# Kernel optimization log

Measured on AMD Instinct MI355X. Metric: run time of the kernel, lower is better.

## Reference

```python
import jax, jax.numpy as jnp
import numpy as np

B, T, C, H, S, M = 4, 4096, 1024, 16, 256, 32
D = C // H  # size_head = 64


def setup_inputs() -> dict:
    key = jax.random.key(0)
    ks = jax.random.split(key, 10)
    scale = 1.0 / (C * C)
    return {
        "x_q": jax.random.normal(ks[0], (B, T, C), dtype=jnp.float32),
        "x_r": jax.random.normal(ks[1], (B, T, C), dtype=jnp.float32),
        "y": jax.random.normal(ks[2], (B, T, C), dtype=jnp.float32),
        "Wi": jax.random.normal(ks[3], (C, C), dtype=jnp.float32) * 0.02,
        "bi": jnp.zeros((C,), jnp.float32),
        "Ws": jax.random.normal(ks[4], (S, D), dtype=jnp.float32) * 0.02,
        "bs": jnp.zeros((S,), jnp.float32),
        "temp": jnp.ones((1, H, 1, 1), jnp.float32) / jnp.sqrt(jnp.float32(D)),
        "w_re": jax.random.uniform(ks[5], (H, D, D, M), dtype=jnp.float32) * scale,
        "w_im": jax.random.uniform(ks[6], (H, D, D, M), dtype=jnp.float32) * scale,
        "Wo": jax.random.normal(ks[7], (C, C), dtype=jnp.float32) * 0.02,
        "bo": jnp.zeros((C,), jnp.float32),
    }


def reference(x_q, x_r, y, Wi, bi, Ws, bs, temp, w_re, w_im, Wo, bo):
    b, t, c = x_q.shape
    d = c // H
    # in_proj -> [B, H, T, D]
    tmp = (x_q @ Wi.T + bi).reshape(b, t, H, d).transpose(0, 2, 1, 3)
    # slice logits [B, H, T, S], scaled by learned temperature
    logits = (tmp @ Ws.T + bs) / temp
    # softmax over tokens (n): slice-attention pooling to S virtual points
    z = jnp.einsum('bhnc,bhns->bhsc', tmp, jax.nn.softmax(logits, axis=-2))
    z = z.transpose(0, 1, 3, 2)  # [B, H, D, S]
    n = z.shape[-1]
    z_fft = jnp.fft.rfft(z)  # [B, H, D, S//2+1]
    w = (w_re + 1j * w_im).astype(z_fft.dtype)
    out_m = jnp.einsum('bhix,hiox->bhox', z_fft[..., :M], w)  # [B, H, D, M]
    out_ft = jnp.zeros((b, H, d, n // 2 + 1), dtype=out_m.dtype).at[..., :M].set(out_m)
    out = jnp.fft.irfft(out_ft, n=n)  # [B, H, D, S]
    out = out.transpose(0, 1, 3, 2)  # [B, H, S, D]
    # softmax over slices (g): scatter back to tokens
    out = jnp.einsum('bhgc,bhng->bhnc', out, jax.nn.softmax(logits, axis=-1))
    out = out.transpose(0, 2, 1, 3).reshape(b, t, c)  # merge heads
    return out @ Wo.T + bo
```

## Files before the change

kernel.cpp:

```cpp
#include <hip/hip_runtime.h>
#include <hip/hip_bf16.h>

typedef __attribute__((ext_vector_type(8))) _Float16 half8;
typedef __attribute__((ext_vector_type(4))) _Float16 half4;
typedef __attribute__((ext_vector_type(4))) float f32x4;

#define DEVFN __device__ __forceinline__

constexpr int B_ = 4, T_ = 4096, C_ = 1024, H_ = 16, S_ = 256, M_ = 32, D_ = 64;
constexpr int NT_ = B_ * T_;
constexpr float FSCALE = 65536.0f;
constexpr float TWOPI = 6.283185307179586f;

DEVFN half8 cvt8(const float4 a, const float4 b) {
  half8 h;
  h[0] = (_Float16)a.x; h[1] = (_Float16)a.y; h[2] = (_Float16)a.z; h[3] = (_Float16)a.w;
  h[4] = (_Float16)b.x; h[5] = (_Float16)b.y; h[6] = (_Float16)b.z; h[7] = (_Float16)b.w;
  return h;
}

#define GLD16(gsrc, ldst)                                                        \
  __builtin_amdgcn_global_load_lds(                                              \
      (const __attribute__((address_space(1))) uint32_t*)(gsrc),                 \
      (__attribute__((address_space(3))) uint32_t*)(ldst), 16, 0, 0)

__global__ void k_diag(float* __restrict__ out, float wsz) {
  if (threadIdx.x == 0 && blockIdx.x == 0) out[0] = wsz;
}

__global__ void kw_cvt(const float* __restrict__ src, _Float16* __restrict__ dst, int n) {
  const int i = (blockIdx.x * blockDim.x + threadIdx.x) * 8;
  if (i < n) {
    float4 a = ((const float4*)(src + i))[0];
    float4 b = ((const float4*)(src + i))[1];
    *(half8*)(dst + i) = cvt8(a, b);
  }
}

__global__ void k0_prep(const float* __restrict__ Ws, const float* __restrict__ bs,
                        const float* __restrict__ temp,
                        _Float16* __restrict__ Wsh, float* __restrict__ bsh) {
  const int h = blockIdx.x;
  const int tid = threadIdx.x;
  const float invt = 1.0f / temp[h];
  for (int i = tid; i < S_ * D_; i += 256)
    Wsh[(size_t)h * S_ * D_ + i] = (_Float16)(Ws[i] * invt);
  if (tid < S_) bsh[h * S_ + tid] = bs[tid] * invt;
}

__global__ __launch_bounds__(256) void k1_in_proj(
    const _Float16* __restrict__ Xh, const _Float16* __restrict__ Wih, const float* __restrict__ bi,
    _Float16* __restrict__ tmp_h, _Float16* __restrict__ tmp_hT)
{
  __shared__ _Float16 As[128 * 32];
  __shared__ _Float16 Bs[128 * 32];
  const int tid = threadIdx.x;
  const int orig = blockIdx.y * gridDim.x + blockIdx.x;
  const int wgid = (orig & 7) * 128 + (orig >> 3);
  const int rowBase = (wgid >> 3) * 128;
  const int colBase = (wgid & 7) * 128;
  const int w = tid >> 6, lane = tid & 63;
  const int wr = w >> 1, wc = w & 1;
  const int fr = lane & 15, fg = lane >> 4;
  const int srow0 = w * 16 + (lane >> 2);
  const int srow1 = (4 + w) * 16 + (lane >> 2);
  const int scol  = (lane & 3) * 8;
  const size_t arow0 = (size_t)(rowBase + srow0) * C_ + scol;
  const size_t arow1 = (size_t)(rowBase + srow1) * C_ + scol;
  const size_t brow0 = (size_t)(colBase + srow0) * C_ + scol;
  const size_t brow1 = (size_t)(colBase + srow1) * C_ + scol;
  f32x4 acc[4][4] = {};
  for (int kt = 0; kt < C_; kt += 32) {
    __syncthreads();
    GLD16(Xh  + arow0 + kt, &As[w * 512]);
    GLD16(Xh  + arow1 + kt, &As[(4 + w) * 512]);
    GLD16(Wih + brow0 + kt, &Bs[w * 512]);
    GLD16(Wih + brow1 + kt, &Bs[(4 + w) * 512]);
    __syncthreads();
    half8 a[4], b[4];
#pragma unroll
    for (int i = 0; i < 4; ++i) a[i] = *(const half8*)&As[(wr * 64 + i * 16 + fr) * 32 + fg * 8];
#pragma unroll
    for (int j = 0; j < 4; ++j) b[j] = *(const half8*)&Bs[(wc * 64 + j * 16 + fr) * 32 + fg * 8];
#pragma unroll
    for (int i = 0; i < 4; ++i)
#pragma unroll
      for (int j = 0; j < 4; ++j)
        acc[i][j] = __builtin_amdgcn_mfma_f32_16x16x32_f16(a[i], b[j], acc[i][j], 0, 0, 0);
  }
#pragma unroll
  for (int i = 0; i < 4; ++i) {
#pragma unroll
    for (int j = 0; j < 4; ++j) {
      const int col = colBase + wc * 64 + j * 16 + fr;
      const int hh = col >> 6, d = col & 63;
      const float bv = bi[col];
      const int g0 = rowBase + wr * 64 + i * 16 + fg * 4;
      const int bb = g0 >> 12;
      const int t0 = g0 & (T_ - 1);
      half4 pk;
#pragma unroll
      for (int r = 0; r < 4; ++r) {
        const _Float16 hv = (_Float16)(acc[i][j][r] + bv);
        tmp_h[(((size_t)(bb * H_ + hh)) * T_ + t0 + r) * D_ + d] = hv;
        pk[r] = hv;
      }
      *(half4*)&tmp_hT[(((size_t)(bb * H_ + hh)) * D_ + d) * T_ + t0] = pk;
    }
  }
}

__global__ __launch_bounds__(256) void k3_pool(
    const _Float16* __restrict__ tmp_h, const _Float16* __restrict__ tmp_hT,
    const _Float16* __restrict__ Wsh, const float* __restrict__ bsh,
    float* __restrict__ Zpart, float* __restrict__ rowsum, float* __restrict__ colsumP)
{
  __shared__ _Float16 Es[256][72];
  __shared__ _Float16 Bt[64][72];
  __shared__ float red[64][4];
  const int tid = threadIdx.x;
  const int kc = blockIdx.x;
  const int bh = blockIdx.y;
  const int hh = bh & (H_ - 1);
  const int w = tid >> 6, lane = tid & 63;
  const int fr = lane & 15, fg = lane >> 4;
  const size_t tmpB  = (size_t)bh * T_ * D_;
  const size_t tmpTB = (size_t)bh * D_ * T_;
  const _Float16* WshH = Wsh + (size_t)hh * S_ * D_;
  float bsreg[4];
#pragma unroll
  for (int nj = 0; nj < 4; ++nj) bsreg[nj] = bsh[hh * S_ + w * 64 + nj * 16 + fr];
  f32x4 acc2[4][4] = {};
  float cacc[4] = {0.f, 0.f, 0.f, 0.f};
  const int brow = tid >> 2, bc0 = (tid & 3) * 16;
  for (int step = 0; step < 8; ++step) {
    const int t0 = kc * 512 + step * 64;
    {
      const _Float16* src = tmp_hT + tmpTB + (size_t)brow * T_ + t0 + bc0;
      *(half8*)&Bt[brow][bc0]     = ((const half8*)src)[0];
      *(half8*)&Bt[brow][bc0 + 8] = ((const half8*)src)[1];
    }
    f32x4 acc1[4][4] = {};
#pragma unroll
    for (int ks = 0; ks < 2; ++ks) {
      half8 a[4], b[4];
#pragma unroll
      for (int mi = 0; mi < 4; ++mi)
        a[mi] = *(const half8*)(tmp_h + tmpB + (size_t)(t0 + mi * 16 + fr) * D_ + ks * 32 + fg * 8);
#pragma unroll
      for (int nj = 0; nj < 4; ++nj)
        b[nj] = *(const half8*)(WshH + (size_t)(w * 64 + nj * 16 + fr) * D_ + ks * 32 + fg * 8);
#pragma unroll
      for (int mi = 0; mi < 4; ++mi)
#pragma unroll
        for (int nj = 0; nj < 4; ++nj)
          acc1[mi][nj] = __builtin_amdgcn_mfma_f32_16x16x32_f16(a[mi], b[nj], acc1[mi][nj], 0, 0, 0);
    }
#pragma unroll
    for (int mi = 0; mi < 4; ++mi) {
      float rsp[4] = {0.f, 0.f, 0.f, 0.f};
#pragma unroll
      for (int nj = 0; nj < 4; ++nj) {
        half4 p;
        float csp = 0.f;
#pragma unroll
        for (int r = 0; r < 4; ++r) {
          const float e = __expf(acc1[mi][nj][r] + bsreg[nj]);
          p[r] = (_Float16)e;
          rsp[r] += e;
          csp += e;
        }
        cacc[nj] += csp;
        *(half4*)&Es[w * 64 + nj * 16 + fr][mi * 16 + fg * 4] = p;
      }
#pragma unroll
      for (int r = 0; r < 4; ++r) {
        float v = rsp[r];
        v += __shfl_xor(v, 1); v += __shfl_xor(v, 2);
        v += __shfl_xor(v, 4); v += __shfl_xor(v, 8);
        if (fr == 0) red[mi * 16 + fg * 4 + r][w] = v;
      }
    }
    __syncthreads();
#pragma unroll
    for (int kt = 0; kt < 2; ++kt) {
      half8 a2[4], b2[4];
#pragma unroll
      for (int mi = 0; mi < 4; ++mi) a2[mi] = *(const half8*)&Es[w * 64 + mi * 16 + fr][kt * 32 + fg * 8];
#pragma unroll
      for (int nj = 0; nj < 4; ++nj) b2[nj] = *(const half8*)&Bt[nj * 16 + fr][kt * 32 + fg * 8];
#pragma unroll
      for (int mi = 0; mi < 4; ++mi)
#pragma unroll
        for (int nj = 0; nj < 4; ++nj)
          acc2[mi][nj] = __builtin_amdgcn_mfma_f32_16x16x32_f16(a2[mi], b2[nj], acc2[mi][nj], 0, 0, 0);
    }
    if (tid < 64)
      rowsum[(size_t)bh * T_ + t0 + tid] = red[tid][0] + red[tid][1] + red[tid][2] + red[tid][3];
    __syncthreads();
  }
#pragma unroll
  for (int nj = 0; nj < 4; ++nj) {
    float v = cacc[nj];
    v += __shfl_xor(v, 16); v += __shfl_xor(v, 32);
    if (fg == 0) colsumP[((size_t)bh * 8 + kc) * S_ + w * 64 + nj * 16 + fr] = v;
  }
#pragma unroll
  for (int mi = 0; mi < 4; ++mi)
#pragma unroll
    for (int nj = 0; nj < 4; ++nj)
#pragma unroll
      for (int r = 0; r < 4; ++r)
        Zpart[(((size_t)bh * 8 + kc) * S_ + w * 64 + mi * 16 + fg * 4 + r) * D_ + nj * 16 + fr]
            = acc2[mi][nj][r];
}

__global__ __launch_bounds__(256) void k4a_dft(
    const float* __restrict__ Zpart, const float* __restrict__ colsumP,
    float* __restrict__ Fre, float* __restrict__ Fim)
{
  __shared__ float zsh[256][17];
  __shared__ float csh[256];
  __shared__ float tc[256], ts[256];
  const int tid = threadIdx.x;
  const int ic = blockIdx.x;
  const int bh = blockIdx.y;
  {
    const float ang = (float)tid * (TWOPI / 256.0f);
    tc[tid] = cosf(ang); ts[tid] = sinf(ang);
    float c = 0.f;
#pragma unroll
    for (int kc = 0; kc < 8; ++kc) c += colsumP[((size_t)bh * 8 + kc) * S_ + tid];
    csh[tid] = c;
  }
  __syncthreads();
  for (int idx = tid; idx < 256 * 16; idx += 256) {
    const int s = idx >> 4, dd = idx & 15;
    float v = 0.f;
#pragma unroll
    for (int kc = 0; kc < 8; ++kc)
      v += Zpart[(((size_t)bh * 8 + kc) * S_ + s) * D_ + ic * 16 + dd];
    zsh[s][dd] = v / csh[s];
  }
  __syncthreads();
  const int ii = tid >> 4;
  const int mh = tid & 15;
#pragma unroll
  for (int q = 0; q < 2; ++q) {
    const int m = mh + 16 * q;
    float re = 0.f, im = 0.f;
    int k = 0;
    for (int s = 0; s < 256; ++s) {
      const float zv = zsh[s][ii];
      re += zv * tc[k];
      im -= zv * ts[k];
      k = (k + m) & 255;
    }
    Fre[((size_t)bh * D_ + ic * 16 + ii) * M_ + m] = re;
    Fim[((size_t)bh * D_ + ic * 16 + ii) * M_ + m] = im;
  }
}

__global__ __launch_bounds__(256) void k4b_mix(
    const float* __restrict__ Fre, const float* __restrict__ Fim,
    const float* __restrict__ w_re, const float* __restrict__ w_im,
    _Float16* __restrict__ fout_T)
{
  __shared__ _Float16 Fsr[4][64][33];
  __shared__ _Float16 Fsi[4][64][33];
  __shared__ float Gpre[2][4][4][32];
  __shared__ float Gpim[2][4][4][32];
  __shared__ float Gre[4][4][32];
  __shared__ float Gim[4][4][32];
  __shared__ float tc[256], ts[256];
  const int tid = threadIdx.x;
  const int oc = blockIdx.x;
  const int h  = blockIdx.y;
  for (int idx = tid; idx < 4 * 64 * 32; idx += 256) {
    const int b = idx >> 11, rem = idx & 2047, i = rem >> 5, m = rem & 31;
    const size_t off = ((size_t)(b * 16 + h) * D_ + i) * M_ + m;
    Fsr[b][i][m] = (_Float16)Fre[off];
    Fsi[b][i][m] = (_Float16)Fim[off];
  }
  {
    const float ang = (float)tid * (TWOPI / 256.0f);
    tc[tid] = cosf(ang); ts[tid] = sinf(ang);
  }
  __syncthreads();
  {
    const int ih = tid >> 7, o = (tid >> 5) & 3, m = tid & 31;
    float gre[4] = {0,0,0,0}, gim[4] = {0,0,0,0};
    for (int i = ih * 32; i < ih * 32 + 32; ++i) {
      const size_t wo = (((size_t)h * D_ + i) * D_ + oc * 4 + o) * M_ + m;
      const float wre = w_re[wo], wim = w_im[wo];
#pragma unroll
      for (int b = 0; b < 4; ++b) {
        const float fre = (float)Fsr[b][i][m], fim = (float)Fsi[b][i][m];
        gre[b] += fre * wre - fim * wim;
        gim[b] += fre * wim + fim * wre;
      }
    }
#pragma unroll
    for (int b = 0; b < 4; ++b) { Gpre[ih][b][o][m] = gre[b]; Gpim[ih][b][o][m] = gim[b]; }
  }
  __syncthreads();
  for (int idx = tid; idx < 512; idx += 256) {
    const int b = idx >> 7, o = (idx >> 5) & 3, m = idx & 31;
    Gre[b][o][m] = Gpre[0][b][o][m] + Gpre[1][b][o][m];
    Gim[b][o][m] = Gpim[0][b][o][m] + Gpim[1][b][o][m];
  }
  __syncthreads();
  {
    const int b = tid >> 6, o = (tid >> 4) & 3, sc = tid & 15;
    for (int s5 = 0; s5 < 16; ++s5) {
      const int s = sc * 16 + s5;
      float v = Gre[b][o][0];
      int km = s;
#pragma unroll
      for (int m = 1; m < 32; ++m) {
        v += 2.0f * (Gre[b][o][m] * tc[km] - Gim[b][o][m] * ts[km]);
        km = (km + s) & 255;
      }
      fout_T[((size_t)(b * 16 + h) * D_ + oc * 4 + o) * S_ + s] = (_Float16)(v * (FSCALE / 256.0f));
    }
  }
}

__global__ __launch_bounds__(256) void k5_scatter(
    const _Float16* __restrict__ Wsh, const float* __restrict__ bsh,
    const _Float16* __restrict__ fout_T, const float* __restrict__ rowsum,
    _Float16* __restrict__ tmp_io)
{
  __shared__ _Float16 Fs[64][264];
  __shared__ _Float16 Es[64][264];
  __shared__ float bshl[256];
  const int tid = threadIdx.x;
  const int orig = blockIdx.y * gridDim.x + blockIdx.x;
  const int nidx = (orig & 7) * 64 + (orig >> 3);
  const int bh = nidx >> 3;
  const int tcn = nidx & 7;
  const int hh = bh & (H_ - 1);
  const int w = tid >> 6, lane = tid & 63;
  const int fr = lane & 15, fg = lane >> 4;
  {
    const int row = tid >> 2, c0 = (tid & 3) * 64;
    const _Float16* src = fout_T + (size_t)bh * D_ * S_ + (size_t)row * S_ + c0;
#pragma unroll
    for (int q = 0; q < 8; ++q)
      *(half8*)&Fs[row][c0 + q * 8] = ((const half8*)src)[q];
  }
  bshl[tid] = bsh[hh * S_ + tid];
  __syncthreads();
  const _Float16* WshH = Wsh + (size_t)hh * S_ * D_;
  const size_t tmpB = (size_t)bh * T_ * D_ + (size_t)tcn * 512 * D_;
  const int trow = w * 16 + fr;
  half8 bf0, bf1;
  {
    const _Float16* p = tmp_io + tmpB + (size_t)trow * D_ + fg * 8;
    bf0 = *(const half8*)p;
    bf1 = *(const half8*)(p + 32);
  }
  for (int step = 0; step < 8; ++step) {
    {
      f32x4 acc1[8];
#pragma unroll
      for (int mi = 0; mi < 8; ++mi) acc1[mi] = (f32x4){0.f, 0.f, 0.f, 0.f};
#pragma unroll
      for (int mi = 0; mi < 8; ++mi) {
        const half8 a0 = *(const half8*)(WshH + (size_t)(mi * 16 + fr) * D_ + fg * 8);
        acc1[mi] = __builtin_amdgcn_mfma_f32_16x16x32_f16(a0, bf0, acc1[mi], 0, 0, 0);
      }
#pragma unroll
      for (int mi = 0; mi < 8; ++mi) {
        const half8 a1 = *(const half8*)(WshH + (size_t)(mi * 16 + fr) * D_ + 32 + fg * 8);
        acc1[mi] = __builtin_amdgcn_mfma_f32_16x16x32_f16(a1, bf1, acc1[mi], 0, 0, 0);
      }
#pragma unroll
      for (int mi = 0; mi < 8; ++mi) {
        const float4 bv = *(const float4*)&bshl[mi * 16 + fg * 4];
        half4 pk;
        pk[0] = (_Float16)__expf(acc1[mi][0] + bv.x);
        pk[1] = (_Float16)__expf(acc1[mi][1] + bv.y);
        pk[2] = (_Float16)__expf(acc1[mi][2] + bv.z);
        pk[3] = (_Float16)__expf(acc1[mi][3] + bv.w);
        *(half4*)&Es[trow][mi * 16 + fg * 4] = pk;
      }
    }
    {
      f32x4 acc1[8];
#pragma unroll
      for (int mi = 0; mi < 8; ++mi) acc1[mi] = (f32x4){0.f, 0.f, 0.f, 0.f};
#pragma unroll
      for (int mi = 0; mi < 8; ++mi) {
        const half8 a0 = *(const half8*)(WshH + (size_t)((8 + mi) * 16 + fr) * D_ + fg * 8);
        acc1[mi] = __builtin_amdgcn_mfma_f32_16x16x32_f16(a0, bf0, acc1[mi], 0, 0, 0);
      }
#pragma unroll
      for (int mi = 0; mi < 8; ++mi) {
        const half8 a1 = *(const half8*)(WshH + (size_t)((8 + mi) * 16 + fr) * D_ + 32 + fg * 8);
        acc1[mi] = __builtin_amdgcn_mfma_f32_16x16x32_f16(a1, bf1, acc1[mi], 0, 0, 0);
      }
#pragma unroll
      for (int mi = 0; mi < 8; ++mi) {
        const float4 bv = *(const float4*)&bshl[(8 + mi) * 16 + fg * 4];
        half4 pk;
        pk[0] = (_Float16)__expf(acc1[mi][0] + bv.x);
        pk[1] = (_Float16)__expf(acc1[mi][1] + bv.y);
        pk[2] = (_Float16)__expf(acc1[mi][2] + bv.z);
        pk[3] = (_Float16)__expf(acc1[mi][3] + bv.w);
        *(half4*)&Es[trow][(8 + mi) * 16 + fg * 4] = pk;
      }
    }
    if (step < 7) {
      const _Float16* p = tmp_io + tmpB + (size_t)((step + 1) * 64 + trow) * D_ + fg * 8;
      bf0 = *(const half8*)p;
      bf1 = *(const half8*)(p + 32);
    }
    f32x4 acc2[4];
#pragma unroll
    for (int nj = 0; nj < 4; ++nj) acc2[nj] = (f32x4){0.f, 0.f, 0.f, 0.f};
#pragma unroll
    for (int ks = 0; ks < 8; ++ks) {
      const half8 ea = *(const half8*)&Es[w * 16 + fr][ks * 32 + fg * 8];
#pragma unroll
      for (int nj = 0; nj < 4; ++nj) {
        const half8 fb = *(const half8*)&Fs[nj * 16 + fr][ks * 32 + fg * 8];
        acc2[nj] = __builtin_amdgcn_mfma_f32_16x16x32_f16(ea, fb, acc2[nj], 0, 0, 0);
      }
    }
    const int tbase = tcn * 512 + step * 64 + w * 16 + fg * 4;
    const float4 rs = *(const float4*)&rowsum[(size_t)bh * T_ + tbase];
    const float ri[4] = {1.0f / rs.x, 1.0f / rs.y, 1.0f / rs.z, 1.0f / rs.w};
#pragma unroll
    for (int r = 0; r < 4; ++r) {
      _Float16* dst = tmp_io + (size_t)bh * T_ * D_ + (size_t)(tbase + r) * D_ + fr;
#pragma unroll
      for (int nj = 0; nj < 4; ++nj)
        dst[nj * 16] = (_Float16)(acc2[nj][r] * ri[r]);
    }
  }
}

__global__ __launch_bounds__(256) void k6_out_proj(
    const _Float16* __restrict__ OT, const _Float16* __restrict__ Woh, const float* __restrict__ bo,
    float* __restrict__ Y)
{
  __shared__ _Float16 As[128 * 32];
  __shared__ _Float16 Bs[128 * 32];
  const int tid = threadIdx.x;
  const int orig = blockIdx.y * gridDim.x + blockIdx.x;
  const int wgid = (orig & 7) * 128 + (orig >> 3);
  const int rowBase = (wgid >> 3) * 128;
  const int colBase = (wgid & 7) * 128;
  const int w = tid >> 6, lane = tid & 63;
  const int wr = w >> 1, wc = w & 1;
  const int fr = lane & 15, fg = lane >> 4;
  const int srow0 = w * 16 + (lane >> 2);
  const int srow1 = (4 + w) * 16 + (lane >> 2);
  const int scol  = (lane & 3) * 8;
  const int g0 = rowBase + srow0, g1 = rowBase + srow1;
  const int bb = g0 >> 12;
  const int t0 = g0 & (T_ - 1), t1 = g1 & (T_ - 1);
  const size_t brow0 = (size_t)(colBase + srow0) * C_ + scol;
  const size_t brow1 = (size_t)(colBase + srow1) * C_ + scol;
  f32x4 acc[4][4] = {};
  for (int kt = 0; kt < C_; kt += 32) {
    const int c0 = kt + scol;
    const int hh0 = c0 >> 6, d0 = c0 & 63;
    __syncthreads();
    GLD16(OT + (((size_t)(bb * H_ + hh0)) * T_ + t0) * D_ + d0, &As[w * 512]);
    GLD16(OT + (((size_t)(bb * H_ + hh0)) * T_ + t1) * D_ + d0, &As[(4 + w) * 512]);
    GLD16(Woh + brow0 + kt, &Bs[w * 512]);
    GLD16(Woh + brow1 + kt, &Bs[(4 + w) * 512]);
    __syncthreads();
    half8 a[4], b[4];
#pragma unroll
    for (int i = 0; i < 4; ++i) a[i] = *(const half8*)&As[(wr * 64 + i * 16 + fr) * 32 + fg * 8];
#pragma unroll
    for (int j = 0; j < 4; ++j) b[j] = *(const half8*)&Bs[(wc * 64 + j * 16 + fr) * 32 + fg * 8];
#pragma unroll
    for (int i = 0; i < 4; ++i)
#pragma unroll
      for (int j = 0; j < 4; ++j)
        acc[i][j] = __builtin_amdgcn_mfma_f32_16x16x32_f16(a[i], b[j], acc[i][j], 0, 0, 0);
  }
#pragma unroll
  for (int i = 0; i < 4; ++i) {
#pragma unroll
    for (int j = 0; j < 4; ++j) {
      const int col = colBase + wc * 64 + j * 16 + fr;
      const float bv = bo[col];
      const int g0o = rowBase + wr * 64 + i * 16 + fg * 4;
#pragma unroll
      for (int r = 0; r < 4; ++r)
        Y[(size_t)(g0o + r) * C_ + col] = acc[i][j][r] * (1.0f / FSCALE) + bv;
    }
  }
}

extern "C" void kernel_launch(void* const* d_in, const int* in_sizes, int n_in,
                              void* d_out, int out_size, void* d_ws, size_t ws_size,
                              hipStream_t stream)
{
  const float* x_q  = (const float*)d_in[0];
  const float* Wi   = (const float*)d_in[3];
  const float* bi   = (const float*)d_in[4];
  const float* Ws   = (const float*)d_in[5];
  const float* bs   = (const float*)d_in[6];
  const float* temp = (const float*)d_in[7];
  const float* w_re = (const float*)d_in[8];
  const float* w_im = (const float*)d_in[9];
  const float* Wo   = (const float*)d_in[10];
  const float* bo   = (const float*)d_in[11];
  float* Y = (float*)d_out;

  char* ws = (char*)d_ws;
  size_t off = 0;
  auto alloc = [&](size_t bytes) { size_t o = off; off += (bytes + 255) & ~(size_t)255; return o; };
  const size_t o_tmp  = alloc((size_t)NT_ * C_ * 2);
  const size_t o_Wsh  = alloc((size_t)H_ * S_ * D_ * 2);
  const size_t o_bsh  = alloc((size_t)H_ * S_ * 4);
  const size_t o_Zp   = alloc((size_t)B_ * H_ * 8 * S_ * D_ * 4);
  const size_t o_row  = alloc((size_t)B_ * H_ * T_ * 4);
  const size_t o_colP = alloc((size_t)B_ * H_ * 8 * S_ * 4);
  const size_t o_Fre  = alloc((size_t)B_ * H_ * D_ * M_ * 4);
  const size_t o_Fim  = alloc((size_t)B_ * H_ * D_ * M_ * 4);
  const size_t o_fout = alloc((size_t)B_ * H_ * D_ * S_ * 2);
  const size_t o_Wih  = alloc((size_t)C_ * C_ * 2);
  const size_t o_Woh  = alloc((size_t)C_ * C_ * 2);
  if (off > ws_size) {
    k_diag<<<1, 64, 0, stream>>>(Y, (float)ws_size);
    return;
  }

  _Float16* tmp    = (_Float16*)(ws + o_tmp);
  _Float16* Wsh    = (_Float16*)(ws + o_Wsh);
  float*    bsh    = (float*)(ws + o_bsh);
  float*    Zpart  = (float*)(ws + o_Zp);
  float*    rowsum = (float*)(ws + o_row);
  float*    colsumP= (float*)(ws + o_colP);
  float*    Fre    = (float*)(ws + o_Fre);
  float*    Fim    = (float*)(ws + o_Fim);
  _Float16* fout_T = (_Float16*)(ws + o_fout);
  _Float16* Wih    = (_Float16*)(ws + o_Wih);
  _Float16* Woh    = (_Float16*)(ws + o_Woh);
  _Float16* Xh     = (_Float16*)d_out;
  _Float16* tmp_hT = (_Float16*)((char*)d_out + (size_t)NT_ * C_ * 2);

  kw_cvt    <<<dim3(8192),    256, 0, stream>>>(x_q, Xh, NT_ * C_);
  kw_cvt    <<<dim3(512),     256, 0, stream>>>(Wi, Wih, C_ * C_);
  kw_cvt    <<<dim3(512),     256, 0, stream>>>(Wo, Woh, C_ * C_);
  k0_prep   <<<dim3(H_),      256, 0, stream>>>(Ws, bs, temp, Wsh, bsh);
  k1_in_proj<<<dim3(8, 128),  256, 0, stream>>>(Xh, Wih, bi, tmp, tmp_hT);
  k3_pool   <<<dim3(8, B_*H_), 256, 0, stream>>>(tmp, tmp_hT, Wsh, bsh, Zpart, rowsum, colsumP);
  k4a_dft   <<<dim3(4, B_*H_), 256, 0, stream>>>(Zpart, colsumP, Fre, Fim);
  k4b_mix   <<<dim3(16, H_),   256, 0, stream>>>(Fre, Fim, w_re, w_im, fout_T);
  k5_scatter<<<dim3(8, B_*H_), 256, 0, stream>>>(Wsh, bsh, fout_T, rowsum, tmp);
  k6_out_proj<<<dim3(8, 128),  256, 0, stream>>>(tmp, Woh, bo, Y);
}
```

Baseline: 328.2 us.

## Widen pool and scatter kernels to 512 threads with double-buffered LDS staging

k3_pool now uses 512 threads and 4 token chunks per head instead of 8, splitting the slice dimension across 8 waves. Token tiles of tmp and tmp^T are double-buffered in shared memory with prefetch, and a block index swizzle is added. k5_scatter is likewise widened to 512 threads with 1024-token chunks. Partial buffers Zpart and colsum shrink to 4 chunks and k4a is updated to match. The grids become 256 blocks each, which may underfill a 256-CU device and raises LDS use per block.

```diff
diff --git a/kernel.cpp b/kernel.cpp
--- a/kernel.cpp
+++ b/kernel.cpp
@@ -110,57 +110,67 @@
   }
 }
 
-__global__ __launch_bounds__(256) void k3_pool(
+__global__ __launch_bounds__(512) void k3_pool(
     const _Float16* __restrict__ tmp_h, const _Float16* __restrict__ tmp_hT,
     const _Float16* __restrict__ Wsh, const float* __restrict__ bsh,
     float* __restrict__ Zpart, float* __restrict__ rowsum, float* __restrict__ colsumP)
 {
+  __shared__ _Float16 At[2][64][72];
+  __shared__ _Float16 Bt[2][64][72];
   __shared__ _Float16 Es[256][72];
-  __shared__ _Float16 Bt[64][72];
-  __shared__ float red[64][4];
-  const int tid = threadIdx.x;
-  const int kc = blockIdx.x;
-  const int bh = blockIdx.y;
+  __shared__ float red[64][8];
+  const int tid = threadIdx.x;
+  const int orig = blockIdx.y * gridDim.x + blockIdx.x;
+  const int nidx = (orig & 7) * 32 + (orig >> 3);
+  const int bh = nidx >> 2;
+  const int kc = nidx & 3;
   const int hh = bh & (H_ - 1);
   const int w = tid >> 6, lane = tid & 63;
   const int fr = lane & 15, fg = lane >> 4;
   const size_t tmpB  = (size_t)bh * T_ * D_;
   const size_t tmpTB = (size_t)bh * D_ * T_;
   const _Float16* WshH = Wsh + (size_t)hh * S_ * D_;
-  float bsreg[4];
-#pragma unroll
-  for (int nj = 0; nj < 4; ++nj) bsreg[nj] = bsh[hh * S_ + w * 64 + nj * 16 + fr];
-  f32x4 acc2[4][4] = {};
-  float cacc[4] = {0.f, 0.f, 0.f, 0.f};
-  const int brow = tid >> 2, bc0 = (tid & 3) * 16;
-  for (int step = 0; step < 8; ++step) {
-    const int t0 = kc * 512 + step * 64;
-    {
-      const _Float16* src = tmp_hT + tmpTB + (size_t)brow * T_ + t0 + bc0;
-      *(half8*)&Bt[brow][bc0]     = ((const half8*)src)[0];
-      *(half8*)&Bt[brow][bc0 + 8] = ((const half8*)src)[1];
-    }
-    f32x4 acc1[4][4] = {};
+  float bsreg[2];
+#pragma unroll
+  for (int nj = 0; nj < 2; ++nj) bsreg[nj] = bsh[hh * S_ + w * 32 + nj * 16 + fr];
+  f32x4 acc2[2][4] = {};
+  float cacc[2] = {0.f, 0.f};
+  const int srow = tid >> 3, sc8 = (tid & 7) * 8;
+  {
+    const int t0 = kc * 1024;
+    *(half8*)&At[0][srow][sc8] = *(const half8*)(tmp_h + tmpB + (size_t)(t0 + srow) * D_ + sc8);
+    *(half8*)&Bt[0][srow][sc8] = *(const half8*)(tmp_hT + tmpTB + (size_t)srow * T_ + t0 + sc8);
+  }
+  for (int step = 0; step < 16; ++step) {
+    const int cur = step & 1, nxt = cur ^ 1;
+    const int t0 = kc * 1024 + step * 64;
+    __syncthreads();
+    f32x4 acc1[4][2] = {};
 #pragma unroll
     for (int ks = 0; ks < 2; ++ks) {
-      half8 a[4], b[4];
+      half8 a[4], b[2];
 #pragma unroll
       for (int mi = 0; mi < 4; ++mi)
-        a[mi] = *(const half8*)(tmp_h + tmpB + (size_t)(t0 + mi * 16 + fr) * D_ + ks * 32 + fg * 8);
-#pragma unroll
-      for (int nj = 0; nj < 4; ++nj)
-        b[nj] = *(const half8*)(WshH + (size_t)(w * 64 + nj * 16 + fr) * D_ + ks * 32 + fg * 8);
+        a[mi] = *(const half8*)&At[cur][mi * 16 + fr][ks * 32 + fg * 8];
+#pragma unroll
+      for (int nj = 0; nj < 2; ++nj)
+        b[nj] = *(const half8*)(WshH + (size_t)(w * 32 + nj * 16 + fr) * D_ + ks * 32 + fg * 8);
 #pragma unroll
       for (int mi = 0; mi < 4; ++mi)
 #pragma unroll
-        for (int nj = 0; nj < 4; ++nj)
+        for (int nj = 0; nj < 2; ++nj)
           acc1[mi][nj] = __builtin_amdgcn_mfma_f32_16x16x32_f16(a[mi], b[nj], acc1[mi][nj], 0, 0, 0);
+    }
+    if (step < 15) {
+      const int t1 = t0 + 64;
+      *(half8*)&At[nxt][srow][sc8] = *(const half8*)(tmp_h + tmpB + (size_t)(t1 + srow) * D_ + sc8);
+      *(half8*)&Bt[nxt][srow][sc8] = *(const half8*)(tmp_hT + tmpTB + (size_t)srow * T_ + t1 + sc8);
     }
 #pragma unroll
     for (int mi = 0; mi < 4; ++mi) {
       float rsp[4] = {0.f, 0.f, 0.f, 0.f};
 #pragma unroll
-      for (int nj = 0; nj < 4; ++nj) {
+      for (int nj = 0; nj < 2; ++nj) {
         half4 p;
         float csp = 0.f;
 #pragma unroll
@@ -171,7 +181,7 @@
           csp += e;
         }
         cacc[nj] += csp;
-        *(half4*)&Es[w * 64 + nj * 16 + fr][mi * 16 + fg * 4] = p;
+        *(half4*)&Es[w * 32 + nj * 16 + fr][mi * 16 + fg * 4] = p;
       }
 #pragma unroll
       for (int r = 0; r < 4; ++r) {
@@ -184,34 +194,36 @@
     __syncthreads();
 #pragma unroll
     for (int kt = 0; kt < 2; ++kt) {
-      half8 a2[4], b2[4];
-#pragma unroll
-      for (int mi = 0; mi < 4; ++mi) a2[mi] = *(const half8*)&Es[w * 64 + mi * 16 + fr][kt * 32 + fg * 8];
-#pragma unroll
-      for (int nj = 0; nj < 4; ++nj) b2[nj] = *(const half8*)&Bt[nj * 16 + fr][kt * 32 + fg * 8];
-#pragma unroll
-      for (int mi = 0; mi < 4; ++mi)
+      half8 a2[2], b2[4];
+#pragma unroll
+      for (int mi = 0; mi < 2; ++mi) a2[mi] = *(const half8*)&Es[w * 32 + mi * 16 + fr][kt * 32 + fg * 8];
+#pragma unroll
+      for (int nj = 0; nj < 4; ++nj) b2[nj] = *(const half8*)&Bt[cur][nj * 16 + fr][kt * 32 + fg * 8];
+#pragma unroll
+      for (int mi = 0; mi < 2; ++mi)
 #pragma unroll
         for (int nj = 0; nj < 4; ++nj)
           acc2[mi][nj] = __builtin_amdgcn_mfma_f32_16x16x32_f16(a2[mi], b2[nj], acc2[mi][nj], 0, 0, 0);
     }
-    if (tid < 64)
-      rowsum[(size_t)bh * T_ + t0 + tid] = red[tid][0] + red[tid][1] + red[tid][2] + red[tid][3];
-    __syncthreads();
-  }
-#pragma unroll
-  for (int nj = 0; nj < 4; ++nj) {
+    if (tid < 64) {
+      const float* rr = red[tid];
+      rowsum[(size_t)bh * T_ + t0 + tid] =
+          rr[0] + rr[1] + rr[2] + rr[3] + rr[4] + rr[5] + rr[6] + rr[7];
+    }
+  }
+#pragma unroll
+  for (int nj = 0; nj < 2; ++nj) {
     float v = cacc[nj];
     v += __shfl_xor(v, 16); v += __shfl_xor(v, 32);
-    if (fg == 0) colsumP[((size_t)bh * 8 + kc) * S_ + w * 64 + nj * 16 + fr] = v;
-  }
-#pragma unroll
-  for (int mi = 0; mi < 4; ++mi)
+    if (fg == 0) colsumP[((size_t)bh * 4 + kc) * S_ + w * 32 + nj * 16 + fr] = v;
+  }
+#pragma unroll
+  for (int mi = 0; mi < 2; ++mi)
 #pragma unroll
     for (int nj = 0; nj < 4; ++nj)
 #pragma unroll
       for (int r = 0; r < 4; ++r)
-        Zpart[(((size_t)bh * 8 + kc) * S_ + w * 64 + mi * 16 + fg * 4 + r) * D_ + nj * 16 + fr]
+        Zpart[(((size_t)bh * 4 + kc) * S_ + w * 32 + mi * 16 + fg * 4 + r) * D_ + nj * 16 + fr]
             = acc2[mi][nj][r];
 }
 
@@ -230,7 +242,7 @@
     tc[tid] = cosf(ang); ts[tid] = sinf(ang);
     float c = 0.f;
 #pragma unroll
-    for (int kc = 0; kc < 8; ++kc) c += colsumP[((size_t)bh * 8 + kc) * S_ + tid];
+    for (int kc = 0; kc < 4; ++kc) c += colsumP[((size_t)bh * 4 + kc) * S_ + tid];
     csh[tid] = c;
   }
   __syncthreads();
@@ -238,8 +250,8 @@
     const int s = idx >> 4, dd = idx & 15;
     float v = 0.f;
 #pragma unroll
-    for (int kc = 0; kc < 8; ++kc)
-      v += Zpart[(((size_t)bh * 8 + kc) * S_ + s) * D_ + ic * 16 + dd];
+    for (int kc = 0; kc < 4; ++kc)
+      v += Zpart[(((size_t)bh * 4 + kc) * S_ + s) * D_ + ic * 16 + dd];
     zsh[s][dd] = v / csh[s];
   }
   __syncthreads();
@@ -326,33 +338,33 @@
   }
 }
 
-__global__ __launch_bounds__(256) void k5_scatter(
+__global__ __launch_bounds__(512) void k5_scatter(
     const _Float16* __restrict__ Wsh, const float* __restrict__ bsh,
     const _Float16* __restrict__ fout_T, const float* __restrict__ rowsum,
     _Float16* __restrict__ tmp_io)
 {
   __shared__ _Float16 Fs[64][264];
-  __shared__ _Float16 Es[64][264];
+  __shared__ _Float16 Es[128][264];
   __shared__ float bshl[256];
   const int tid = threadIdx.x;
   const int orig = blockIdx.y * gridDim.x + blockIdx.x;
-  const int nidx = (orig & 7) * 64 + (orig >> 3);
-  const int bh = nidx >> 3;
-  const int tcn = nidx & 7;
+  const int nidx = (orig & 7) * 32 + (orig >> 3);
+  const int bh = nidx >> 2;
+  const int tcn = nidx & 3;
   const int hh = bh & (H_ - 1);
   const int w = tid >> 6, lane = tid & 63;
   const int fr = lane & 15, fg = lane >> 4;
   {
-    const int row = tid >> 2, c0 = (tid & 3) * 64;
+    const int row = tid >> 3, c0 = (tid & 7) * 32;
     const _Float16* src = fout_T + (size_t)bh * D_ * S_ + (size_t)row * S_ + c0;
 #pragma unroll
-    for (int q = 0; q < 8; ++q)
+    for (int q = 0; q < 4; ++q)
       *(half8*)&Fs[row][c0 + q * 8] = ((const half8*)src)[q];
   }
-  bshl[tid] = bsh[hh * S_ + tid];
+  if (tid < 256) bshl[tid] = bsh[hh * S_ + tid];
   __syncthreads();
   const _Float16* WshH = Wsh + (size_t)hh * S_ * D_;
-  const size_t tmpB = (size_t)bh * T_ * D_ + (size_t)tcn * 512 * D_;
+  const size_t tmpB = (size_t)bh * T_ * D_ + (size_t)tcn * 1024 * D_;
   const int trow = w * 16 + fr;
   half8 bf0, bf1;
   {
@@ -412,7 +424,7 @@
       }
     }
     if (step < 7) {
-      const _Float16* p = tmp_io + tmpB + (size_t)((step + 1) * 64 + trow) * D_ + fg * 8;
+      const _Float16* p = tmp_io + tmpB + (size_t)((step + 1) * 128 + trow) * D_ + fg * 8;
       bf0 = *(const half8*)p;
       bf1 = *(const half8*)(p + 32);
     }
@@ -428,7 +440,7 @@
         acc2[nj] = __builtin_amdgcn_mfma_f32_16x16x32_f16(ea, fb, acc2[nj], 0, 0, 0);
       }
     }
-    const int tbase = tcn * 512 + step * 64 + w * 16 + fg * 4;
+    const int tbase = tcn * 1024 + step * 128 + w * 16 + fg * 4;
     const float4 rs = *(const float4*)&rowsum[(size_t)bh * T_ + tbase];
     const float ri[4] = {1.0f / rs.x, 1.0f / rs.y, 1.0f / rs.z, 1.0f / rs.w};
 #pragma unroll
@@ -520,9 +532,9 @@
   const size_t o_tmp  = alloc((size_t)NT_ * C_ * 2);
   const size_t o_Wsh  = alloc((size_t)H_ * S_ * D_ * 2);
   const size_t o_bsh  = alloc((size_t)H_ * S_ * 4);
-  const size_t o_Zp   = alloc((size_t)B_ * H_ * 8 * S_ * D_ * 4);
+  const size_t o_Zp   = alloc((size_t)B_ * H_ * 4 * S_ * D_ * 4);
   const size_t o_row  = alloc((size_t)B_ * H_ * T_ * 4);
-  const size_t o_colP = alloc((size_t)B_ * H_ * 8 * S_ * 4);
+  const size_t o_colP = alloc((size_t)B_ * H_ * 4 * S_ * 4);
   const size_t o_Fre  = alloc((size_t)B_ * H_ * D_ * M_ * 4);
   const size_t o_Fim  = alloc((size_t)B_ * H_ * D_ * M_ * 4);
   const size_t o_fout = alloc((size_t)B_ * H_ * D_ * S_ * 2);
@@ -552,9 +564,9 @@
   kw_cvt    <<<dim3(512),     256, 0, stream>>>(Wo, Woh, C_ * C_);
   k0_prep   <<<dim3(H_),      256, 0, stream>>>(Ws, bs, temp, Wsh, bsh);
   k1_in_proj<<<dim3(8, 128),  256, 0, stream>>>(Xh, Wih, bi, tmp, tmp_hT);
-  k3_pool   <<<dim3(8, B_*H_), 256, 0, stream>>>(tmp, tmp_hT, Wsh, bsh, Zpart, rowsum, colsumP);
+  k3_pool   <<<dim3(4, B_*H_), 512, 0, stream>>>(tmp, tmp_hT, Wsh, bsh, Zpart, rowsum, colsumP);
   k4a_dft   <<<dim3(4, B_*H_), 256, 0, stream>>>(Zpart, colsumP, Fre, Fim);
   k4b_mix   <<<dim3(16, H_),   256, 0, stream>>>(Fre, Fim, w_re, w_im, fout_T);
-  k5_scatter<<<dim3(8, B_*H_), 256, 0, stream>>>(Wsh, bsh, fout_T, rowsum, tmp);
+  k5_scatter<<<dim3(4, B_*H_), 512, 0, stream>>>(Wsh, bsh, fout_T, rowsum, tmp);
   k6_out_proj<<<dim3(8, 128),  256, 0, stream>>>(tmp, Woh, bo, Y);
 }
```

New measurement: 356.3 us. +8.5%, slower.

## Remove block barriers in pooling kernel via per-wave partial row sums

Applied to the files above, without the earlier changes.

The pooling kernel no longer stages the transposed tmp tile in shared memory. Each wave now reads its MFMA B operands directly from global memory, and it writes per-wave partial row sums to a new workspace buffer. That removes both __syncthreads per step and the shared-memory reduction. The four partial row sums are combined later in the DFT kernel. The trade is more global traffic (every wave loads the B tile, and the partials are written and read back) in exchange for no block-level synchronisation. One risk: the Es tile is written and read by the same wave with no barrier, which is only safe if each wave reads only its own rows.

```diff
diff --git a/kernel.cpp b/kernel.cpp
--- a/kernel.cpp
+++ b/kernel.cpp
@@ -113,11 +113,9 @@
 __global__ __launch_bounds__(256) void k3_pool(
     const _Float16* __restrict__ tmp_h, const _Float16* __restrict__ tmp_hT,
     const _Float16* __restrict__ Wsh, const float* __restrict__ bsh,
-    float* __restrict__ Zpart, float* __restrict__ rowsum, float* __restrict__ colsumP)
+    float* __restrict__ Zpart, float* __restrict__ rowsumP, float* __restrict__ colsumP)
 {
   __shared__ _Float16 Es[256][72];
-  __shared__ _Float16 Bt[64][72];
-  __shared__ float red[64][4];
   const int tid = threadIdx.x;
   const int kc = blockIdx.x;
   const int bh = blockIdx.y;
@@ -132,14 +130,8 @@
   for (int nj = 0; nj < 4; ++nj) bsreg[nj] = bsh[hh * S_ + w * 64 + nj * 16 + fr];
   f32x4 acc2[4][4] = {};
   float cacc[4] = {0.f, 0.f, 0.f, 0.f};
-  const int brow = tid >> 2, bc0 = (tid & 3) * 16;
   for (int step = 0; step < 8; ++step) {
     const int t0 = kc * 512 + step * 64;
-    {
-      const _Float16* src = tmp_hT + tmpTB + (size_t)brow * T_ + t0 + bc0;
-      *(half8*)&Bt[brow][bc0]     = ((const half8*)src)[0];
-      *(half8*)&Bt[brow][bc0 + 8] = ((const half8*)src)[1];
-    }
     f32x4 acc1[4][4] = {};
 #pragma unroll
     for (int ks = 0; ks < 2; ++ks) {
@@ -178,26 +170,28 @@
         float v = rsp[r];
         v += __shfl_xor(v, 1); v += __shfl_xor(v, 2);
         v += __shfl_xor(v, 4); v += __shfl_xor(v, 8);
-        if (fr == 0) red[mi * 16 + fg * 4 + r][w] = v;
-      }
-    }
-    __syncthreads();
+        rsp[r] = v;
+      }
+      if (fr == 0) {
+        float4 rv; rv.x = rsp[0]; rv.y = rsp[1]; rv.z = rsp[2]; rv.w = rsp[3];
+        *(float4*)&rowsumP[((size_t)(bh * 4 + w)) * T_ + t0 + mi * 16 + fg * 4] = rv;
+      }
+    }
 #pragma unroll
     for (int kt = 0; kt < 2; ++kt) {
       half8 a2[4], b2[4];
 #pragma unroll
-      for (int mi = 0; mi < 4; ++mi) a2[mi] = *(const half8*)&Es[w * 64 + mi * 16 + fr][kt * 32 + fg * 8];
-#pragma unroll
-      for (int nj = 0; nj < 4; ++nj) b2[nj] = *(const half8*)&Bt[nj * 16 + fr][kt * 32 + fg * 8];
+      for (int mi = 0; mi < 4; ++mi)
+        a2[mi] = *(const half8*)&Es[w * 64 + mi * 16 + fr][kt * 32 + fg * 8];
+#pragma unroll
+      for (int nj = 0; nj < 4; ++nj)
+        b2[nj] = *(const half8*)(tmp_hT + tmpTB + (size_t)(nj * 16 + fr) * T_ + t0 + kt * 32 + fg * 8);
 #pragma unroll
       for (int mi = 0; mi < 4; ++mi)
 #pragma unroll
         for (int nj = 0; nj < 4; ++nj)
           acc2[mi][nj] = __builtin_amdgcn_mfma_f32_16x16x32_f16(a2[mi], b2[nj], acc2[mi][nj], 0, 0, 0);
     }
-    if (tid < 64)
-      rowsum[(size_t)bh * T_ + t0 + tid] = red[tid][0] + red[tid][1] + red[tid][2] + red[tid][3];
-    __syncthreads();
   }
 #pragma unroll
   for (int nj = 0; nj < 4; ++nj) {
@@ -217,7 +211,8 @@
 
 __global__ __launch_bounds__(256) void k4a_dft(
     const float* __restrict__ Zpart, const float* __restrict__ colsumP,
-    float* __restrict__ Fre, float* __restrict__ Fim)
+    const float* __restrict__ rowsumP,
+    float* __restrict__ Fre, float* __restrict__ Fim, float* __restrict__ rowsum)
 {
   __shared__ float zsh[256][17];
   __shared__ float csh[256];
@@ -225,6 +220,15 @@
   const int tid = threadIdx.x;
   const int ic = blockIdx.x;
   const int bh = blockIdx.y;
+#pragma unroll
+  for (int q = 0; q < 4; ++q) {
+    const int t = ic * 1024 + q * 256 + tid;
+    float v = rowsumP[((size_t)(bh * 4 + 0)) * T_ + t]
+            + rowsumP[((size_t)(bh * 4 + 1)) * T_ + t]
+            + rowsumP[((size_t)(bh * 4 + 2)) * T_ + t]
+            + rowsumP[((size_t)(bh * 4 + 3)) * T_ + t];
+    rowsum[(size_t)bh * T_ + t] = v;
+  }
   {
     const float ang = (float)tid * (TWOPI / 256.0f);
     tc[tid] = cosf(ang); ts[tid] = sinf(ang);
@@ -522,6 +526,7 @@
   const size_t o_bsh  = alloc((size_t)H_ * S_ * 4);
   const size_t o_Zp   = alloc((size_t)B_ * H_ * 8 * S_ * D_ * 4);
   const size_t o_row  = alloc((size_t)B_ * H_ * T_ * 4);
+  const size_t o_rowP = alloc((size_t)B_ * H_ * 4 * T_ * 4);
   const size_t o_colP = alloc((size_t)B_ * H_ * 8 * S_ * 4);
   const size_t o_Fre  = alloc((size_t)B_ * H_ * D_ * M_ * 4);
   const size_t o_Fim  = alloc((size_t)B_ * H_ * D_ * M_ * 4);
@@ -538,6 +543,7 @@
   float*    bsh    = (float*)(ws + o_bsh);
   float*    Zpart  = (float*)(ws + o_Zp);
   float*    rowsum = (float*)(ws + o_row);
+  float*    rowsumP= (float*)(ws + o_rowP);
   float*    colsumP= (float*)(ws + o_colP);
   float*    Fre    = (float*)(ws + o_Fre);
   float*    Fim    = (float*)(ws + o_Fim);
@@ -552,8 +558,8 @@
   kw_cvt    <<<dim3(512),     256, 0, stream>>>(Wo, Woh, C_ * C_);
   k0_prep   <<<dim3(H_),      256, 0, stream>>>(Ws, bs, temp, Wsh, bsh);
   k1_in_proj<<<dim3(8, 128),  256, 0, stream>>>(Xh, Wih, bi, tmp, tmp_hT);
-  k3_pool   <<<dim3(8, B_*H_), 256, 0, stream>>>(tmp, tmp_hT, Wsh, bsh, Zpart, rowsum, colsumP);
-  k4a_dft   <<<dim3(4, B_*H_), 256, 0, stream>>>(Zpart, colsumP, Fre, Fim);
+  k3_pool   <<<dim3(8, B_*H_), 256, 0, stream>>>(tmp, tmp_hT, Wsh, bsh, Zpart, rowsumP, colsumP);
+  k4a_dft   <<<dim3(4, B_*H_), 256, 0, stream>>>(Zpart, colsumP, rowsumP, Fre, Fim, rowsum);
   k4b_mix   <<<dim3(16, H_),   256, 0, stream>>>(Fre, Fim, w_re, w_im, fout_T);
   k5_scatter<<<dim3(8, B_*H_), 256, 0, stream>>>(Wsh, bsh, fout_T, rowsum, tmp);
   k6_out_proj<<<dim3(8, 128),  256, 0, stream>>>(tmp, Woh, bo, Y);
```

Measured after the change: 298.6 us. 1.1x faster.
